# Performance work log

Measured on AMD Instinct MI355X. Metric: run time of the kernel, lower is better.

## Reference

```python
import jax, jax.numpy as jnp
import numpy as np

N_NODES = 50000
N_EDGES = 1600000
N_GRAPHS = 512
IN_DIM = 64
HID = 128
OUT_DIM = 10


def setup_inputs() -> dict:
    key = jax.random.key(0)
    ks = jax.random.split(key, 12)
    x = jax.random.normal(ks[0], (N_NODES, IN_DIM), dtype=jnp.float32)
    edge_index = jax.random.randint(ks[1], (2, N_EDGES), 0, N_NODES, dtype=jnp.int64)
    batch = jnp.sort(jax.random.randint(ks[2], (N_NODES,), 0, N_GRAPHS, dtype=jnp.int64))
    edge_attr = jax.random.uniform(ks[3], (N_EDGES,), dtype=jnp.float32)
    # glorot-ish init for weights
    def lin(k, fan_in, fan_out):
        s = (6.0 / (fan_in + fan_out)) ** 0.5
        return jax.random.uniform(k, (fan_in, fan_out), minval=-s, maxval=s, dtype=jnp.float32)
    return {
        "x": x, "edge_index": edge_index, "batch": batch, "edge_attr": edge_attr,
        "W1": lin(ks[4], IN_DIM, HID), "b1": jnp.zeros((HID,), jnp.float32),
        "W2": lin(ks[5], HID, HID), "b2": jnp.zeros((HID,), jnp.float32),
        "Wm1": lin(ks[6], HID, HID), "bm1": jnp.zeros((HID,), jnp.float32),
        "Wm2": lin(ks[7], HID, OUT_DIM), "bm2": jnp.zeros((OUT_DIM,), jnp.float32),
    }


def _gcn_conv(x, edge_index, edge_weight, W, b, num_nodes):
    """PyG GCNConv: add self-loops, symmetric norm with edge weights, x@W, scatter-add, +bias."""
    loop = jnp.arange(num_nodes, dtype=edge_index.dtype)
    src = jnp.concatenate([edge_index[0], loop])
    dst = jnp.concatenate([edge_index[1], loop])
    ew = jnp.concatenate([edge_weight, jnp.ones((num_nodes,), edge_weight.dtype)])
    deg = jax.ops.segment_sum(ew, dst, num_segments=num_nodes)  # [N]
    dinv = jnp.where(deg > 0, jax.lax.rsqrt(jnp.where(deg > 0, deg, 1.0)), 0.0)
    norm = dinv[src] * ew * dinv[dst]  # [E+N]
    h = x @ W  # [N, F_out]
    msg = h[src] * norm[:, None]  # gather + scale
    out = jax.ops.segment_sum(msg, dst, num_segments=num_nodes)
    return out + b


def reference(x, edge_index, batch, edge_attr, W1, b1, W2, b2, Wm1, bm1, Wm2, bm2):
    n = x.shape[0]
    h = _gcn_conv(x, edge_index, edge_attr, W1, b1, n)
    h = jax.nn.relu(h)  # dropout = identity in eval mode
    h = _gcn_conv(h, edge_index, edge_attr, W2, b2, n)
    h = jax.nn.relu(h)
    pooled = jax.ops.segment_sum(h, batch, num_segments=N_GRAPHS)  # global_add_pool
    z = jax.nn.relu(pooled @ Wm1 + bm1)
    return z @ Wm2 + bm2  # [num_graphs, out_dim]
```

## Files before the change

### kernel.cpp

```cpp
#include <hip/hip_runtime.h>
#include <hip/hip_bf16.h>
#include <hip/hip_fp16.h>
#include <cstdint>

#define HIDC 128
#define FIXSCALE 4194304.0f
#define FIXINV   (1.0f / 4194304.0f)
#define MAXDEG 80

#define BKT_SHIFT 7
#define BKT_NODES 128
#define BKT_CAP   4608
#define BIN_TILE  4096
#define BIN_THREADS 512

typedef _Float16 half8 __attribute__((ext_vector_type(8)));
typedef float float4v __attribute__((ext_vector_type(4)));

__global__ __launch_bounds__(256) void prep_kernel(
        const float* __restrict__ W1, const float* __restrict__ W2,
        _Float16* __restrict__ W1t, _Float16* __restrict__ W2t,
        unsigned int* __restrict__ tails, int nbkt) {
    int i = blockIdx.x * 256 + threadIdx.x;
    if (i < 16384) { int k = i >> 7, n = i & 127; W2t[n * 128 + k] = (_Float16)W2[i]; }
    if (i < 8192)  { int k = i >> 7, n = i & 127; W1t[n * 64 + k]  = (_Float16)W1[i]; }
    if (i < nbkt) tails[i] = 0u;
}

__global__ __launch_bounds__(BIN_THREADS) void bin_kernel(
        const int* __restrict__ ei, const float* __restrict__ ea,
        unsigned int* __restrict__ buck_lo, unsigned char* __restrict__ buck_dl,
        unsigned int* __restrict__ tails, int E, int nbkt) {
    __shared__ unsigned long long rec[BIN_TILE];
    __shared__ unsigned int cnt[BIN_THREADS];
    __shared__ unsigned int startx[BIN_THREADS];
    __shared__ unsigned int cur[BIN_THREADS];
    __shared__ unsigned int gbase[BIN_THREADS];
    __shared__ unsigned int wtot[BIN_THREADS / 64];
    int t = threadIdx.x;
    int base = blockIdx.x * BIN_TILE;
    int total = E - base; if (total > BIN_TILE) total = BIN_TILE;

    cnt[t] = 0;
    __syncthreads();

    unsigned int lo[8], dv[8];
#pragma unroll
    for (int j = 0; j < 8; ++j) {
        int e = base + j * BIN_THREADS + t;
        if (e < E) {
            int s = ei[e]; int d = ei[E + e]; float w = ea[e];
            lo[j] = (unsigned int)s |
                    ((unsigned int)__half_as_ushort(__float2half_rn(w)) << 16);
            dv[j] = (unsigned int)d;
            atomicAdd(&cnt[dv[j] >> BKT_SHIFT], 1u);
        } else dv[j] = 0xffffffffu;
    }
    __syncthreads();

    unsigned int c = cnt[t];
    unsigned int sc = c;
#pragma unroll
    for (int off = 1; off < 64; off <<= 1) {
        unsigned int v = __shfl_up(sc, off);
        if ((t & 63) >= off) sc += v;
    }
    if ((t & 63) == 63) wtot[t >> 6] = sc;
    __syncthreads();
    unsigned int wbase = 0;
    int w = t >> 6;
    for (int i = 0; i < w; ++i) wbase += wtot[i];
    unsigned int excl = sc + wbase - c;
    startx[t] = excl;
    cur[t] = excl;
    if (t < nbkt) gbase[t] = atomicAdd(&tails[t], c);
    __syncthreads();

#pragma unroll
    for (int j = 0; j < 8; ++j) {
        if (dv[j] != 0xffffffffu) {
            unsigned int p = atomicAdd(&cur[dv[j] >> BKT_SHIFT], 1u);
            rec[p] = ((unsigned long long)dv[j] << 32) | (unsigned long long)lo[j];
        }
    }
    __syncthreads();

    for (int i = t; i < total; i += BIN_THREADS) {
        unsigned long long r = rec[i];
        unsigned int hi = (unsigned int)(r >> 32);
        unsigned int b = hi >> BKT_SHIFT;
        unsigned int idx = gbase[b] + ((unsigned int)i - startx[b]);
        if (idx < BKT_CAP) {
            buck_lo[b * BKT_CAP + idx] = (unsigned int)r;
            buck_dl[b * BKT_CAP + idx] = (unsigned char)(hi & (BKT_NODES - 1));
        }
    }
}

__global__ __launch_bounds__(256) void fill_kernel(
        const unsigned int* __restrict__ buck_lo,
        const unsigned char* __restrict__ buck_dl,
        const unsigned int* __restrict__ tails,
        const float* __restrict__ x,
        unsigned long long* __restrict__ degcnt,
        unsigned int* __restrict__ padcsr,
        _Float16* __restrict__ xt, int n_nodes) {
    __shared__ unsigned long long deg[BKT_NODES];
    __shared__ float sdinv[BKT_NODES];
    int b = blockIdx.x, t = threadIdx.x;
    if (t < BKT_NODES) deg[t] = 0ull;
    __syncthreads();
    int cnt_b = (int)tails[b]; if (cnt_b > BKT_CAP) cnt_b = BKT_CAP;
    unsigned int boff = (unsigned int)b * BKT_CAP;
    int nodeBase = b << BKT_SHIFT;
    for (int i = t; i < cnt_b; i += 256) {
        unsigned int lo = buck_lo[boff + i];
        unsigned int dl = buck_dl[boff + i];
        float w = __half2float(__ushort_as_half((unsigned short)(lo >> 16)));
        unsigned int fx = (unsigned int)(w * FIXSCALE + 0.5f);
        unsigned long long old =
            atomicAdd(&deg[dl], (1ull << 32) | (unsigned long long)fx);
        unsigned int rank = (unsigned int)(old >> 32);
        if (rank < MAXDEG)
            padcsr[(size_t)(nodeBase + dl) * MAXDEG + rank] = lo;
    }
    __syncthreads();
    if (t < BKT_NODES) {
        unsigned long long dv = deg[t];
        sdinv[t] = rsqrtf(1.0f + (float)(unsigned int)(dv & 0xffffffffull) * FIXINV);
        int node = nodeBase + t;
        if (node < n_nodes) {
            degcnt[node] = dv;
            int cw = (int)(dv >> 32); if (cw > MAXDEG) cw = MAXDEG;
            int cp = (cw + 7) & ~7;
            for (int r = cw; r < cp; ++r)
                padcsr[(size_t)node * MAXDEG + r] = 0u;
        }
    }
    __syncthreads();
    int d = t & 63, nl = t >> 6;
    for (int nn = nl; nn < BKT_NODES; nn += 4) {
        int node = nodeBase + nn;
        if (node < n_nodes)
            xt[(size_t)node * 64 + d] = (_Float16)(x[(size_t)node * 64 + d] * sdinv[nn]);
    }
}

__global__ __launch_bounds__(256) void agg0_kernel(
        const _Float16* __restrict__ xt,
        const unsigned long long* __restrict__ degcnt,
        const unsigned int* __restrict__ padcsr,
        _Float16* __restrict__ g, int n_nodes) {
    int wave = threadIdx.x >> 6, lane = threadIdx.x & 63;
    int node = blockIdx.x * 4 + wave;
    if (node >= n_nodes) return;
    int qd = lane >> 3, li = lane & 7;
    unsigned long long v = degcnt[node];
    int cnt = (int)(v >> 32); if (cnt > MAXDEG) cnt = MAXDEG;
    int cntp = (cnt + 7) & ~7;
    float di = rsqrtf(1.0f + (float)(unsigned int)(v & 0xffffffffull) * FIXINV);
    const unsigned int* row = padcsr + (size_t)node * MAXDEG;
    unsigned base_li = (unsigned)(li * 8);
    float acc[8];
#pragma unroll
    for (int k = 0; k < 8; ++k) acc[k] = 0.f;
    int e = 0;
    for (; e + 32 <= cntp; e += 32) {
        unsigned int p[4];
#pragma unroll
        for (int j = 0; j < 4; ++j) p[j] = row[e + 8 * j + qd];
        uint4 vv[4];
#pragma unroll
        for (int j = 0; j < 4; ++j)
            vv[j] = *reinterpret_cast<const uint4*>(
                xt + (p[j] & 0xffffu) * 64u + base_li);
#pragma unroll
        for (int j = 0; j < 4; ++j) {
            __half ch = __ushort_as_half((unsigned short)(p[j] >> 16));
            float cf = __half2float(ch);
            const __half2* hp = reinterpret_cast<const __half2*>(&vv[j]);
#pragma unroll
            for (int k = 0; k < 4; ++k) {
                float2 f = __half22float2(hp[k]);
                acc[2 * k]     = fmaf(cf, f.x, acc[2 * k]);
                acc[2 * k + 1] = fmaf(cf, f.y, acc[2 * k + 1]);
            }
        }
    }
    for (; e < cntp; e += 8) {
        unsigned int p = row[e + qd];
        uint4 vv = *reinterpret_cast<const uint4*>(
            xt + (p & 0xffffu) * 64u + base_li);
        __half ch = __ushort_as_half((unsigned short)(p >> 16));
        float cf = __half2float(ch);
        const __half2* hp = reinterpret_cast<const __half2*>(&vv);
#pragma unroll
        for (int k = 0; k < 4; ++k) {
            float2 f = __half22float2(hp[k]);
            acc[2 * k]     = fmaf(cf, f.x, acc[2 * k]);
            acc[2 * k + 1] = fmaf(cf, f.y, acc[2 * k + 1]);
        }
    }
#pragma unroll
    for (int k = 0; k < 8; ++k) {
        acc[k] += __shfl_xor(acc[k], 8);
        acc[k] += __shfl_xor(acc[k], 16);
        acc[k] += __shfl_xor(acc[k], 32);
    }
    if (qd == 0) {
        uint4 sv = *reinterpret_cast<const uint4*>(
            xt + (unsigned)node * 64u + base_li);
        const __half2* sp = reinterpret_cast<const __half2*>(&sv);
        __half2 o[4];
#pragma unroll
        for (int k = 0; k < 4; ++k) {
            float2 f = __half22float2(sp[k]);
            o[k] = __floats2half2_rn(di * (acc[2 * k] + f.x),
                                     di * (acc[2 * k + 1] + f.y));
        }
        uint4 st;
        st.x = *reinterpret_cast<unsigned int*>(&o[0]);
        st.y = *reinterpret_cast<unsigned int*>(&o[1]);
        st.z = *reinterpret_cast<unsigned int*>(&o[2]);
        st.w = *reinterpret_cast<unsigned int*>(&o[3]);
        *reinterpret_cast<uint4*>(g + (size_t)node * 64 + base_li) = st;
    }
}

__global__ __launch_bounds__(256) void agg2_kernel(const __half* __restrict__ h,
                                                   const unsigned long long* __restrict__ degcnt,
                                                   const unsigned int* __restrict__ padcsr,
                                                   __half* __restrict__ out, int n_nodes) {
    int wave = threadIdx.x >> 6, lane = threadIdx.x & 63;
    int node = blockIdx.x * 4 + wave;
    if (node >= n_nodes) return;
    int qd = lane >> 4, li = lane & 15;
    unsigned long long v = degcnt[node];
    int cnt = (int)(v >> 32); if (cnt > MAXDEG) cnt = MAXDEG;
    int cntp = (cnt + 7) & ~7;
    float di = rsqrtf(1.0f + (float)(unsigned int)(v & 0xffffffffull) * FIXINV);
    const unsigned int* row = padcsr + (size_t)node * MAXDEG;
    unsigned base_li = (unsigned)(li * 8);
    float acc[8];
#pragma unroll
    for (int k = 0; k < 8; ++k) acc[k] = 0.f;
    int e = 0;
    for (; e + 32 <= cntp; e += 32) {
        unsigned int p[8];
#pragma unroll
        for (int j = 0; j < 8; ++j) p[j] = row[e + 4 * j + qd];
        uint4 vv[8];
#pragma unroll
        for (int j = 0; j < 8; ++j)
            vv[j] = *reinterpret_cast<const uint4*>(
                h + (p[j] & 0xffffu) * 128u + base_li);
#pragma unroll
        for (int j = 0; j < 8; ++j) {
            __half ch = __ushort_as_half((unsigned short)(p[j] >> 16));
            float cf = __half2float(ch);
            const __half2* hp = reinterpret_cast<const __half2*>(&vv[j]);
#pragma unroll
            for (int k = 0; k < 4; ++k) {
                float2 f = __half22float2(hp[k]);
                acc[2 * k]     = fmaf(cf, f.x, acc[2 * k]);
                acc[2 * k + 1] = fmaf(cf, f.y, acc[2 * k + 1]);
            }
        }
    }
    for (; e < cntp; e += 8) {
        unsigned int p[2];
#pragma unroll
        for (int j = 0; j < 2; ++j) p[j] = row[e + 4 * j + qd];
        uint4 vv[2];
#pragma unroll
        for (int j = 0; j < 2; ++j)
            vv[j] = *reinterpret_cast<const uint4*>(
                h + (p[j] & 0xffffu) * 128u + base_li);
#pragma unroll
        for (int j = 0; j < 2; ++j) {
            __half ch = __ushort_as_half((unsigned short)(p[j] >> 16));
            float cf = __half2float(ch);
            const __half2* hp = reinterpret_cast<const __half2*>(&vv[j]);
#pragma unroll
            for (int k = 0; k < 4; ++k) {
                float2 f = __half22float2(hp[k]);
                acc[2 * k]     = fmaf(cf, f.x, acc[2 * k]);
                acc[2 * k + 1] = fmaf(cf, f.y, acc[2 * k + 1]);
            }
        }
    }
#pragma unroll
    for (int k = 0; k < 8; ++k) {
        acc[k] += __shfl_xor(acc[k], 16);
        acc[k] += __shfl_xor(acc[k], 32);
    }
    if (qd == 0) {
        uint4 sv = *reinterpret_cast<const uint4*>(
            h + (unsigned)node * 128u + base_li);
        const __half2* sp = reinterpret_cast<const __half2*>(&sv);
        __half2 o[4];
#pragma unroll
        for (int k = 0; k < 4; ++k) {
            float2 f = __half22float2(sp[k]);
            o[k] = __floats2half2_rn(di * (acc[2 * k] + f.x),
                                     di * (acc[2 * k + 1] + f.y));
        }
        uint4 st;
        st.x = *reinterpret_cast<unsigned int*>(&o[0]);
        st.y = *reinterpret_cast<unsigned int*>(&o[1]);
        st.z = *reinterpret_cast<unsigned int*>(&o[2]);
        st.w = *reinterpret_cast<unsigned int*>(&o[3]);
        *reinterpret_cast<uint4*>(out + (size_t)node * 128 + base_li) = st;
    }
}

__global__ __launch_bounds__(256) void gemm1_mfma_kernel(
        const _Float16* __restrict__ G,
        const _Float16* __restrict__ W1t,
        const float* __restrict__ b1,
        const unsigned long long* __restrict__ degcnt,
        __half* __restrict__ out, int n_nodes) {
    int wave = threadIdx.x >> 6, lane = threadIdx.x & 63;
    int nodeBase = (blockIdx.x * 4 + wave) * 16;
    if (nodeBase >= n_nodes) return;
    int mrow = lane & 15, quad = lane >> 4;

    int anode = nodeBase + mrow; if (anode >= n_nodes) anode = n_nodes - 1;
    const _Float16* Arow = G + (size_t)anode * 64 + quad * 8;
    half8 a[2];
    a[0] = *(const half8*)(Arow);
    a[1] = *(const half8*)(Arow + 32);

    float4v acc[8];
#pragma unroll
    for (int nt = 0; nt < 8; ++nt) acc[nt] = (float4v)(0.f);
#pragma unroll
    for (int nt = 0; nt < 8; ++nt) {
        const _Float16* Brow = W1t + (size_t)(nt * 16 + mrow) * 64 + quad * 8;
#pragma unroll
        for (int q = 0; q < 2; ++q) {
            half8 b = *(const half8*)(Brow + q * 32);
            acc[nt] = __builtin_amdgcn_mfma_f32_16x16x32_f16(a[q], b, acc[nt], 0, 0, 0);
        }
    }
#pragma unroll
    for (int r = 0; r < 4; ++r) {
        int node = nodeBase + quad * 4 + r;
        if (node < n_nodes) {
            unsigned long long v = degcnt[node];
            float di = rsqrtf(1.0f + (float)(unsigned int)(v & 0xffffffffull) * FIXINV);
#pragma unroll
            for (int nt = 0; nt < 8; ++nt) {
                int col = nt * 16 + mrow;
                float val = fmaxf(acc[nt][r] + b1[col], 0.f) * di;
                out[(size_t)node * 128 + col] = __float2half(val);
            }
        }
    }
}

__global__ __launch_bounds__(256) void gemm2_mfma_kernel(
        const __half* __restrict__ A,
        const _Float16* __restrict__ W2t,
        const float* __restrict__ b2,
        __half* __restrict__ out, int n_nodes) {
    int wave = threadIdx.x >> 6, lane = threadIdx.x & 63;
    int nodeBase = (blockIdx.x * 4 + wave) * 16;
    if (nodeBase >= n_nodes) return;
    int mrow = lane & 15, quad = lane >> 4;

    int anode = nodeBase + mrow; if (anode >= n_nodes) anode = n_nodes - 1;
    const _Float16* Arow = (const _Float16*)A + (size_t)anode * 128 + quad * 8;
    half8 a[4];
#pragma unroll
    for (int q = 0; q < 4; ++q) a[q] = *(const half8*)(Arow + q * 32);

    float4v acc[8];
#pragma unroll
    for (int nt = 0; nt < 8; ++nt) acc[nt] = (float4v)(0.f);
#pragma unroll
    for (int nt = 0; nt < 8; ++nt) {
        const _Float16* Brow = W2t + (size_t)(nt * 16 + mrow) * 128 + quad * 8;
#pragma unroll
        for (int q = 0; q < 4; ++q) {
            half8 b = *(const half8*)(Brow + q * 32);
            acc[nt] = __builtin_amdgcn_mfma_f32_16x16x32_f16(a[q], b, acc[nt], 0, 0, 0);
        }
    }
#pragma unroll
    for (int r = 0; r < 4; ++r) {
        int node = nodeBase + quad * 4 + r;
        if (node < n_nodes) {
#pragma unroll
            for (int nt = 0; nt < 8; ++nt) {
                int col = nt * 16 + mrow;
                float val = fmaxf(acc[nt][r] + b2[col], 0.f);
                out[(size_t)node * 128 + col] = __float2half(val);
            }
        }
    }
}

__global__ __launch_bounds__(256) void pool_mlp_kernel(const __half* __restrict__ h,
                                                       const int* __restrict__ batch,
                                                       const float* __restrict__ Wm1,
                                                       const float* __restrict__ bm1,
                                                       const float* __restrict__ Wm2,
                                                       const float* __restrict__ bm2,
                                                       float* __restrict__ out,
                                                       int n_nodes, int out_dim) {
    int g = blockIdx.x;
    int t = threadIdx.x;
    __shared__ int sb[2];
    __shared__ float row2[256];
    __shared__ float row[128];
    __shared__ float zl[128];
    if (t < 2) {
        int target = g + t;
        int lo = 0, hi = n_nodes;
        while (lo < hi) { int mid = (lo + hi) >> 1; if (batch[mid] < target) lo = mid + 1; else hi = mid; }
        sb[t] = lo;
    }
    __syncthreads();
    int beg = sb[0], end = sb[1];
    int dim = t & 127, sub = t >> 7;
    float p = 0.f;
    for (int i = beg + sub; i < end; i += 2)
        p += __half2float(h[(size_t)i * 128 + dim]);
    row2[t] = p;
    __syncthreads();
    if (t < 128) row[t] = row2[t] + row2[t + 128];
    __syncthreads();
    if (t < 128) {
        float acc = bm1[t];
#pragma unroll 8
        for (int k = 0; k < 128; ++k) acc += row[k] * Wm1[k * 128 + t];
        zl[t] = fmaxf(acc, 0.f);
    }
    __syncthreads();
    if (t < out_dim) {
        float o = bm2[t];
#pragma unroll 8
        for (int k = 0; k < 128; ++k) o += zl[k] * Wm2[k * out_dim + t];
        out[g * out_dim + t] = o;
    }
}

extern "C" void kernel_launch(void* const* d_in, const int* in_sizes, int n_in,
                              void* d_out, int out_size, void* d_ws, size_t ws_size,
                              hipStream_t stream) {
    const float* x   = (const float*)d_in[0];
    const int*   ei  = (const int*)d_in[1];
    const int*   bat = (const int*)d_in[2];
    const float* ea  = (const float*)d_in[3];
    const float* W1  = (const float*)d_in[4];
    const float* b1  = (const float*)d_in[5];
    const float* W2  = (const float*)d_in[6];
    const float* b2  = (const float*)d_in[7];
    const float* Wm1 = (const float*)d_in[8];
    const float* bm1 = (const float*)d_in[9];
    const float* Wm2 = (const float*)d_in[10];
    const float* bm2 = (const float*)d_in[11];
    float* out = (float*)d_out;

    const int N = in_sizes[2];
    const int E = in_sizes[1] / 2;
    const int N_GRAPHS = 512;
    const int OUT_DIM = out_size / N_GRAPHS;

    char* ws = (char*)d_ws;
    size_t off = 0;
    auto alloc = [&](size_t bytes) { char* p = ws + off; off += (bytes + 255) & ~size_t(255); return p; };
    char* regB = alloc((size_t)N * HIDC * 2);
    char* regC = alloc((size_t)N * HIDC * 2);
    char* regA = alloc((size_t)N * MAXDEG * 4);
    unsigned long long* degcnt = (unsigned long long*)alloc((size_t)N * 8);
    _Float16* W2t = (_Float16*)alloc(128 * 128 * 2);
    _Float16* W1t = (_Float16*)alloc(128 * 64 * 2);
    unsigned int* tails = (unsigned int*)alloc(BIN_THREADS * 4);

    int nbkt = (N + BKT_NODES - 1) >> BKT_SHIFT;
    unsigned int*  buck_lo = (unsigned int*)regB;
    unsigned char* buck_dl = (unsigned char*)(regB + (size_t)nbkt * BKT_CAP * 4);
    __half*    htld = (__half*)regB;
    _Float16*  xt   = (_Float16*)regC;
    _Float16*  gbuf = (_Float16*)(regC + (size_t)N * 64 * 2);
    __half*    ubuf = (__half*)regC;
    unsigned int* padcsr = (unsigned int*)regA;
    __half*    zbuf = (__half*)regA;

    prep_kernel<<<64, 256, 0, stream>>>(W1, W2, W1t, W2t, tails, nbkt);
    int binBlocks = (E + BIN_TILE - 1) / BIN_TILE;
    bin_kernel<<<binBlocks, BIN_THREADS, 0, stream>>>(ei, ea, buck_lo, buck_dl, tails, E, nbkt);
    fill_kernel<<<nbkt, 256, 0, stream>>>(buck_lo, buck_dl, tails, x, degcnt, padcsr, xt, N);
    agg0_kernel<<<(N + 3) / 4, 256, 0, stream>>>(xt, degcnt, padcsr, gbuf, N);
    gemm1_mfma_kernel<<<(N + 63) / 64, 256, 0, stream>>>(gbuf, W1t, b1, degcnt, htld, N);
    agg2_kernel<<<(N + 3) / 4, 256, 0, stream>>>(htld, degcnt, padcsr, ubuf, N);
    gemm2_mfma_kernel<<<(N + 63) / 64, 256, 0, stream>>>(ubuf, W2t, b2, zbuf, N);
    pool_mlp_kernel<<<N_GRAPHS, 256, 0, stream>>>(zbuf, bat, Wm1, bm1, Wm2, bm2, out, N, OUT_DIM);
}
```

Measured before the change: 263.2 us.

## Fuse global add pooling into second GEMM via atomic adds

The second-layer GEMM epilogue now atomically accumulates ReLU outputs directly into a per-graph pooled fp32 buffer instead of writing a half-precision node feature matrix. The pool kernel becomes a small MLP-only kernel that reads the pooled rows. This removes a full write and reread of the layer-2 activations and the binary search per graph. The cost is millions of float atomics concentrated on few addresses, plus a memset, and nondeterministic summation order.

```diff
diff --git a/kernel.cpp b/kernel.cpp
--- a/kernel.cpp
+++ b/kernel.cpp
@@ -359,11 +359,12 @@
     }
 }
 
-__global__ __launch_bounds__(256) void gemm2_mfma_kernel(
+__global__ __launch_bounds__(256) void gemm2_pool_kernel(
         const __half* __restrict__ A,
         const _Float16* __restrict__ W2t,
         const float* __restrict__ b2,
-        __half* __restrict__ out, int n_nodes) {
+        const int* __restrict__ batch,
+        float* __restrict__ pooled, int n_nodes) {
     int wave = threadIdx.x >> 6, lane = threadIdx.x & 63;
     int nodeBase = (blockIdx.x * 4 + wave) * 16;
     if (nodeBase >= n_nodes) return;
@@ -391,52 +392,34 @@
     for (int r = 0; r < 4; ++r) {
         int node = nodeBase + quad * 4 + r;
         if (node < n_nodes) {
+            float* pg = pooled + (size_t)batch[node] * 128;
 #pragma unroll
             for (int nt = 0; nt < 8; ++nt) {
                 int col = nt * 16 + mrow;
                 float val = fmaxf(acc[nt][r] + b2[col], 0.f);
-                out[(size_t)node * 128 + col] = __float2half(val);
+                atomicAdd(&pg[col], val);
             }
         }
     }
 }
 
-__global__ __launch_bounds__(256) void pool_mlp_kernel(const __half* __restrict__ h,
-                                                       const int* __restrict__ batch,
-                                                       const float* __restrict__ Wm1,
-                                                       const float* __restrict__ bm1,
-                                                       const float* __restrict__ Wm2,
-                                                       const float* __restrict__ bm2,
-                                                       float* __restrict__ out,
-                                                       int n_nodes, int out_dim) {
+__global__ __launch_bounds__(128) void mlp_kernel(const float* __restrict__ pooled,
+                                                  const float* __restrict__ Wm1,
+                                                  const float* __restrict__ bm1,
+                                                  const float* __restrict__ Wm2,
+                                                  const float* __restrict__ bm2,
+                                                  float* __restrict__ out,
+                                                  int out_dim) {
     int g = blockIdx.x;
     int t = threadIdx.x;
-    __shared__ int sb[2];
-    __shared__ float row2[256];
     __shared__ float row[128];
     __shared__ float zl[128];
-    if (t < 2) {
-        int target = g + t;
-        int lo = 0, hi = n_nodes;
-        while (lo < hi) { int mid = (lo + hi) >> 1; if (batch[mid] < target) lo = mid + 1; else hi = mid; }
-        sb[t] = lo;
-    }
-    __syncthreads();
-    int beg = sb[0], end = sb[1];
-    int dim = t & 127, sub = t >> 7;
-    float p = 0.f;
-    for (int i = beg + sub; i < end; i += 2)
-        p += __half2float(h[(size_t)i * 128 + dim]);
-    row2[t] = p;
-    __syncthreads();
-    if (t < 128) row[t] = row2[t] + row2[t + 128];
-    __syncthreads();
-    if (t < 128) {
-        float acc = bm1[t];
+    row[t] = pooled[(size_t)g * 128 + t];
+    __syncthreads();
+    float acc = bm1[t];
 #pragma unroll 8
-        for (int k = 0; k < 128; ++k) acc += row[k] * Wm1[k * 128 + t];
-        zl[t] = fmaxf(acc, 0.f);
-    }
+    for (int k = 0; k < 128; ++k) acc += row[k] * Wm1[k * 128 + t];
+    zl[t] = fmaxf(acc, 0.f);
     __syncthreads();
     if (t < out_dim) {
         float o = bm2[t];
@@ -478,6 +461,7 @@
     _Float16* W2t = (_Float16*)alloc(128 * 128 * 2);
     _Float16* W1t = (_Float16*)alloc(128 * 64 * 2);
     unsigned int* tails = (unsigned int*)alloc(BIN_THREADS * 4);
+    float* pooled = (float*)alloc((size_t)N_GRAPHS * 128 * 4);
 
     int nbkt = (N + BKT_NODES - 1) >> BKT_SHIFT;
     unsigned int*  buck_lo = (unsigned int*)regB;
@@ -487,8 +471,8 @@
     _Float16*  gbuf = (_Float16*)(regC + (size_t)N * 64 * 2);
     __half*    ubuf = (__half*)regC;
     unsigned int* padcsr = (unsigned int*)regA;
-    __half*    zbuf = (__half*)regA;
-
+
+    hipMemsetAsync(pooled, 0, (size_t)N_GRAPHS * 128 * 4, stream);
     prep_kernel<<<64, 256, 0, stream>>>(W1, W2, W1t, W2t, tails, nbkt);
     int binBlocks = (E + BIN_TILE - 1) / BIN_TILE;
     bin_kernel<<<binBlocks, BIN_THREADS, 0, stream>>>(ei, ea, buck_lo, buck_dl, tails, E, nbkt);
@@ -496,6 +480,6 @@
     agg0_kernel<<<(N + 3) / 4, 256, 0, stream>>>(xt, degcnt, padcsr, gbuf, N);
     gemm1_mfma_kernel<<<(N + 63) / 64, 256, 0, stream>>>(gbuf, W1t, b1, degcnt, htld, N);
     agg2_kernel<<<(N + 3) / 4, 256, 0, stream>>>(htld, degcnt, padcsr, ubuf, N);
-    gemm2_mfma_kernel<<<(N + 63) / 64, 256, 0, stream>>>(ubuf, W2t, b2, zbuf, N);
-    pool_mlp_kernel<<<N_GRAPHS, 256, 0, stream>>>(zbuf, bat, Wm1, bm1, Wm2, bm2, out, N, OUT_DIM);
-}
+    gemm2_pool_kernel<<<(N + 63) / 64, 256, 0, stream>>>(ubuf, W2t, b2, bat, pooled, N);
+    mlp_kernel<<<N_GRAPHS, 128, 0, stream>>>(pooled, Wm1, bm1, Wm2, bm2, out, OUT_DIM);
+}
```

Measured after the change: 322.0 us. 22.3% more time.
